# Optimization experiments

Measured on AMD Instinct MI355X. Metric: run time of the kernel, lower is better.

The kernel has to match this reference:

```python
import jax, jax.numpy as jnp
import numpy as np

EMBED = 256
HID = 256          # LSTM hidden_dim
ENC = 256          # enc_hid_dim
DEC = 256          # dec_hid_dim (attention)


def setup_inputs() -> dict:
    key = jax.random.key(0)
    ks = jax.random.split(key, 8)
    T, B, S = 256, 128, 512
    sc = 0.05
    return {
        "tgt": jax.random.normal(ks[0], (T, B, EMBED), dtype=jnp.float32),
        "memory": jax.random.normal(ks[1], (S, B, ENC), dtype=jnp.float32),
        # attention: Linear(enc+dec -> dec), input cat order = (hidden, encoder)
        "W_attn": jax.random.normal(ks[2], (DEC, DEC + ENC), dtype=jnp.float32) * sc,
        "b_attn": jnp.zeros((DEC,), dtype=jnp.float32),
        # LSTM (1 layer): input = embed + enc = 512, gates order i,f,g,o
        "W_ih": jax.random.normal(ks[3], (4 * HID, EMBED + ENC), dtype=jnp.float32) * sc,
        "W_hh": jax.random.normal(ks[4], (4 * HID, HID), dtype=jnp.float32) * sc,
        "b_ih": jnp.zeros((4 * HID,), dtype=jnp.float32),
        "b_hh": jnp.zeros((4 * HID,), dtype=jnp.float32),
    }


def _decode_scan(tgt, memory, W_attn, b_attn, W_ih, W_hh, b_ih, b_hh):
    T, B, _ = tgt.shape
    mem_bt = jnp.transpose(memory, (1, 0, 2))           # [B, S, ENC]
    # split attention weight by cat order (hidden first, then encoder)
    W_h = W_attn[:, :DEC]                               # [DEC, DEC]
    W_m = W_attn[:, DEC:]                               # [DEC, ENC]
    # precompute the memory side of the attention projection once
    mem_proj = jnp.einsum('bse,de->bsd', mem_bt, W_m) + b_attn  # [B, S, DEC]

    def step(carry, emb_t):
        h, c = carry                                    # [B, HID] each
        # Bahdanau attention: tanh(W[h; m]) summed over feature dim, softmax over S
        energy = jnp.tanh(mem_proj + (h @ W_h.T)[:, None, :])    # [B, S, DEC]
        attn = jax.nn.softmax(energy.sum(-1), axis=1)            # [B, S]
        ctx = jnp.einsum('bs,bse->be', attn, mem_bt)             # [B, ENC]
        x = jnp.concatenate([emb_t, ctx], axis=-1)               # [B, EMBED+ENC]
        gates = x @ W_ih.T + h @ W_hh.T + (b_ih + b_hh)          # [B, 4H]
        i, f, g, o = jnp.split(gates, 4, axis=-1)
        i, f, o = jax.nn.sigmoid(i), jax.nn.sigmoid(f), jax.nn.sigmoid(o)
        c_new = f * c + i * jnp.tanh(g)
        h_new = o * jnp.tanh(c_new)
        return (h_new, c_new), h_new

    h0 = jnp.zeros((B, HID), dtype=tgt.dtype)
    c0 = jnp.zeros((B, HID), dtype=tgt.dtype)
    # loop runs for t = 1..T-1; outputs[0] stays zero, tgt[0] unused
    _, outs = jax.lax.scan(step, (h0, c0), tgt[1:])              # [T-1, B, HID]
    return jnp.concatenate([jnp.zeros((1, B, HID), dtype=tgt.dtype), outs], axis=0)


def reference(tgt, memory, W_attn, b_attn, W_ih, W_hh, b_ih, b_hh):
    return _decode_scan(tgt, memory, W_attn, b_attn, W_ih, W_hh, b_ih, b_hh)
```

## Files before the change

kernel.cpp:

```cpp
#include <hip/hip_runtime.h>
#include <string.h>

#define T_STEPS 256
#define B_SZ    128
#define S_SZ    512
#define D_SZ    256
#define NG      1024

__device__ float g_proj[(size_t)B_SZ * S_SZ * 256];
__device__ float g_E[(size_t)T_STEPS * B_SZ * 1024];
__device__ float g_WihT[512 * 1024];
__device__ float g_WhhT[256 * 1024];
__device__ float g_WhT [256 * 256];
__device__ float g_WmT [256 * 256];
__device__ float g_bias[1024];

__device__ __forceinline__ float tanh_f(float x){
    float r = __expf(2.f * x);
    return 1.f - 2.f / (r + 1.f);
}
__device__ __forceinline__ float sigm_f(float x){
    return 1.f / (1.f + __expf(-x));
}


__global__ void pack_attn(const float* __restrict__ W_attn){
    int id = blockIdx.x * 256 + threadIdx.x;
    int d = id >> 8, k = id & 255;
    g_WhT[k * 256 + d] = W_attn[d * 512 + k];
    g_WmT[k * 256 + d] = W_attn[d * 512 + 256 + k];
}

__global__ void pack_wih(const float* __restrict__ W){
    int id = blockIdx.x * 256 + threadIdx.x;
    int j = id >> 9, k = id & 511;
    g_WihT[k * 1024 + j] = W[id];
}
__global__ void pack_whh(const float* __restrict__ W){
    int id = blockIdx.x * 256 + threadIdx.x;
    int j = id >> 8, k = id & 255;
    g_WhhT[k * 1024 + j] = W[id];
}
__global__ void pack_bias(const float* __restrict__ bih, const float* __restrict__ bhh){
    int j = blockIdx.x * 256 + threadIdx.x;
    g_bias[j] = bih[j] + bhh[j];
}

#define PBM 64
#define PBN 64
#define PBK 32
__global__ __launch_bounds__(256) void mem_proj_gemm(
        const float* __restrict__ memory,
        const float* __restrict__ b_attn){
    __shared__ float As[PBK][PBM + 1];
    __shared__ float Bs[PBK][PBN + 1];
    int tid = threadIdx.x;
    int tm = tid >> 4, tn = tid & 15;
    int row0 = blockIdx.x * PBM;
    int col0 = blockIdx.y * PBN;
    float acc[4][4] = {};
    for (int k0 = 0; k0 < 256; k0 += PBK){
        int m = tid >> 2, kq = tid & 3;
        int r  = row0 + m;
        int bb = r >> 9, ss = r & 511;
        const float* ap = memory + ((size_t)ss * B_SZ + bb) * 256 + k0 + kq * 8;
        #pragma unroll
        for (int i = 0; i < 8; ++i) As[kq * 8 + i][m] = ap[i];
        int kk = tid >> 3, dq = tid & 7;
        const float* bp = g_WmT + (size_t)(k0 + kk) * 256 + col0 + dq * 8;
        #pragma unroll
        for (int i = 0; i < 8; ++i) Bs[kk][dq * 8 + i] = bp[i];
        __syncthreads();
        #pragma unroll
        for (int k2 = 0; k2 < PBK; ++k2){
            float a[4], bb2[4];
            #pragma unroll
            for (int i = 0; i < 4; ++i) a[i]   = As[k2][tm * 4 + i];
            #pragma unroll
            for (int i = 0; i < 4; ++i) bb2[i] = Bs[k2][tn * 4 + i];
            #pragma unroll
            for (int i = 0; i < 4; ++i)
                #pragma unroll
                for (int j = 0; j < 4; ++j) acc[i][j] += a[i] * bb2[j];
        }
        __syncthreads();
    }
    #pragma unroll
    for (int i = 0; i < 4; ++i){
        int r = row0 + tm * 4 + i;
        float* pp = g_proj + (size_t)r * 256 + col0 + tn * 4;
        #pragma unroll
        for (int j = 0; j < 4; ++j)
            pp[j] = acc[i][j] + b_attn[col0 + tn * 4 + j];
    }
}

__global__ __launch_bounds__(256) void emb_gemm(
        const float* __restrict__ tgt){
    __shared__ float As[PBK][PBM + 1];
    __shared__ float Bs[PBK][PBN + 1];
    int tid = threadIdx.x;
    int tm = tid >> 4, tn = tid & 15;
    int row0 = blockIdx.x * PBM;
    int col0 = blockIdx.y * PBN;
    float acc[4][4] = {};
    for (int k0 = 0; k0 < 256; k0 += PBK){
        int m = tid >> 2, kq = tid & 3;
        const float* ap = tgt + (size_t)(row0 + m) * 256 + k0 + kq * 8;
        #pragma unroll
        for (int i = 0; i < 8; ++i) As[kq * 8 + i][m] = ap[i];
        int kk = tid >> 3, dq = tid & 7;
        const float* bp = g_WihT + (size_t)(k0 + kk) * 1024 + col0 + dq * 8;
        #pragma unroll
        for (int i = 0; i < 8; ++i) Bs[kk][dq * 8 + i] = bp[i];
        __syncthreads();
        #pragma unroll
        for (int k2 = 0; k2 < PBK; ++k2){
            float a[4], bb2[4];
            #pragma unroll
            for (int i = 0; i < 4; ++i) a[i]   = As[k2][tm * 4 + i];
            #pragma unroll
            for (int i = 0; i < 4; ++i) bb2[i] = Bs[k2][tn * 4 + i];
            #pragma unroll
            for (int i = 0; i < 4; ++i)
                #pragma unroll
                for (int j = 0; j < 4; ++j) acc[i][j] += a[i] * bb2[j];
        }
        __syncthreads();
    }
    #pragma unroll
    for (int i = 0; i < 4; ++i){
        int r = row0 + tm * 4 + i;
        float* pp = g_E + (size_t)r * 1024 + col0 + tn * 4;
        #pragma unroll
        for (int j = 0; j < 4; ++j)
            __builtin_nontemporal_store(acc[i][j], pp + j);
    }
}

__global__ __launch_bounds__(1024) void decode_scan(
        const float* __restrict__ memory,
        float* __restrict__ out)
{
    const int b    = blockIdx.x;
    const int tid  = threadIdx.x;
    const int lane = tid & 63;
    const int wave = tid >> 6;

    __shared__ __align__(16) float h_s[256];
    __shared__ __align__(16) float c_s[256];
    __shared__ __align__(16) float hWh_part[4][256];
    __shared__ __align__(16) float hWh[256];
    __shared__ __align__(16) float e_s[512];
    __shared__ __align__(16) float attn[512];
    __shared__ __align__(16) float ctx_part[16][256];
    __shared__ __align__(16) float ctx_s[256];
    __shared__ __align__(16) float g_part[4][1024];
    __shared__ __align__(16) float gates[1024];

    if (tid < 256){
        h_s[tid] = 0.f; c_s[tid] = 0.f;
        __builtin_nontemporal_store(0.f, out + (size_t)b * 256 + tid);
    }
    __syncthreads();

    const float* projb = g_proj + (size_t)b * S_SZ * 256;
    const float* memb  = memory + (size_t)b * 256;

    for (int t = 1; t < T_STEPS; ++t){
        {
            int d = tid & 255, kq = tid >> 8;
            float acc = 0.f;
            const float* wp = g_WhT + (size_t)(kq * 64) * 256 + d;
            #pragma unroll 8
            for (int k = 0; k < 64; ++k)
                acc += h_s[kq * 64 + k] * wp[(size_t)k * 256];
            hWh_part[kq][d] = acc;
        }
        __syncthreads();
        if (tid < 256)
            hWh[tid] = hWh_part[0][tid] + hWh_part[1][tid] + hWh_part[2][tid] + hWh_part[3][tid];
        __syncthreads();

        {
            float4 hv = ((const float4*)hWh)[lane];
            for (int i = 0; i < 32; ++i){
                int s = wave * 32 + i;
                float4 p = ((const float4*)(projb + (size_t)s * 256))[lane];
                float v = tanh_f(p.x + hv.x) + tanh_f(p.y + hv.y)
                        + tanh_f(p.z + hv.z) + tanh_f(p.w + hv.w);
                #pragma unroll
                for (int m = 32; m; m >>= 1) v += __shfl_xor(v, m, 64);
                if (lane == 0) e_s[s] = v;
            }
        }
        __syncthreads();

        if (wave == 0){
            float v[8]; float mx = -1e30f;
            #pragma unroll
            for (int i = 0; i < 8; ++i){ v[i] = e_s[lane + 64 * i]; mx = fmaxf(mx, v[i]); }
            #pragma unroll
            for (int m = 32; m; m >>= 1) mx = fmaxf(mx, __shfl_xor(mx, m, 64));
            float zs = 0.f;
            #pragma unroll
            for (int i = 0; i < 8; ++i){ v[i] = __expf(v[i] - mx); zs += v[i]; }
            #pragma unroll
            for (int m = 32; m; m >>= 1) zs += __shfl_xor(zs, m, 64);
            float inv = 1.f / zs;
            #pragma unroll
            for (int i = 0; i < 8; ++i) attn[lane + 64 * i] = v[i] * inv;
        }
        __syncthreads();

        {
            int e4 = tid & 63, sq = tid >> 6;
            float a0=0.f, a1=0.f, a2=0.f, a3=0.f;
            const float* mp = memb + (size_t)(sq * 32) * 32768 + 4 * e4;
            #pragma unroll 4
            for (int s = 0; s < 32; ++s){
                float av = attn[sq * 32 + s];
                float4 w = *(const float4*)(mp + (size_t)s * 32768);
                a0 += av * w.x; a1 += av * w.y;
                a2 += av * w.z; a3 += av * w.w;
            }
            float4 r; r.x=a0; r.y=a1; r.z=a2; r.w=a3;
            ((float4*)ctx_part[sq])[e4] = r;
        }
        __syncthreads();
        if (tid < 256){
            float s = 0.f;
            #pragma unroll
            for (int g = 0; g < 16; ++g) s += ctx_part[g][tid];
            ctx_s[tid] = s;
        }
        __syncthreads();

        {
            int jq = tid & 255, kh = tid >> 8;
            float a0=0.f, a1=0.f, a2=0.f, a3=0.f;
            const float* src;
            const float* wp;
            if (kh < 2){
                src = ctx_s + kh * 128;
                wp  = g_WihT + (size_t)(256 + kh * 128) * 1024 + 4 * jq;
            } else {
                src = h_s + (kh - 2) * 128;
                wp  = g_WhhT + (size_t)((kh - 2) * 128) * 1024 + 4 * jq;
            }
            #pragma unroll 4
            for (int k = 0; k < 128; ++k){
                float xv = src[k];
                float4 w = *(const float4*)(wp + (size_t)k * 1024);
                a0 += xv * w.x; a1 += xv * w.y;
                a2 += xv * w.z; a3 += xv * w.w;
            }
            float4 r; r.x=a0; r.y=a1; r.z=a2; r.w=a3;
            ((float4*)g_part[kh])[jq] = r;
        }
        __syncthreads();
        {
            const float* Erow = g_E + ((size_t)t * B_SZ + b) * 1024;
            float ev = __builtin_nontemporal_load(Erow + tid);
            gates[tid] = g_part[0][tid] + g_part[1][tid] + g_part[2][tid]
                       + g_part[3][tid] + ev + g_bias[tid];
        }
        __syncthreads();

        if (tid < 256){
            float ig = sigm_f(gates[tid]);
            float fg = sigm_f(gates[256 + tid]);
            float gg = tanh_f(gates[512 + tid]);
            float og = sigm_f(gates[768 + tid]);
            float cn = fg * c_s[tid] + ig * gg;
            float hn = og * tanh_f(cn);
            c_s[tid] = cn; h_s[tid] = hn;
            __builtin_nontemporal_store(hn, out + ((size_t)t * B_SZ + b) * 256 + tid);
        }
        __syncthreads();
    }
}

extern "C" void kernel_launch(void* const* d_in, const int* in_sizes, int n_in,
                              void* d_out, int out_size, void* d_ws, size_t ws_size,
                              hipStream_t stream){
    const float* tgt    = (const float*)d_in[0];
    const float* memory = (const float*)d_in[1];
    const float* W_attn = (const float*)d_in[2];
    const float* b_attn = (const float*)d_in[3];
    const float* W_ih   = (const float*)d_in[4];
    const float* W_hh   = (const float*)d_in[5];
    const float* b_ih   = (const float*)d_in[6];
    const float* b_hh   = (const float*)d_in[7];
    float* out = (float*)d_out;
    (void)d_ws; (void)ws_size; (void)in_sizes; (void)n_in; (void)out_size;

    pack_attn<<<256, 256, 0, stream>>>(W_attn);
    pack_wih<<<2048, 256, 0, stream>>>(W_ih);
    pack_whh<<<1024, 256, 0, stream>>>(W_hh);
    pack_bias<<<4, 256, 0, stream>>>(b_ih, b_hh);
    emb_gemm<<<dim3(512, 16), 256, 0, stream>>>(tgt);
    mem_proj_gemm<<<dim3(1024, 4), 256, 0, stream>>>(memory, b_attn);
    decode_scan<<<128, 1024, 0, stream>>>(memory, out);
}
```

Baseline: 14.70 ms.

## Split each batch row's decode across two cooperating blocks with flag sync

The recurrent decode kernel now uses two 512-thread blocks per batch element. Each block handles half of the source positions for attention energy and context, and half of the gate columns. Partial energies, contexts and gates are exchanged through global memory, with three spin-flag pair syncs per timestep. The aim is to use 256 CUs instead of 128 and halve per-block work. The cost is cross-block synchronization latency, and the spin cap means results could silently go wrong if the partner block is not co-resident.

```diff
diff --git a/kernel.cpp b/kernel.cpp
--- a/kernel.cpp
+++ b/kernel.cpp
@@ -6,6 +6,8 @@
 #define S_SZ    512
 #define D_SZ    256
 #define NG      1024
+
+#define SPIN_CAP 50000
 
 __device__ float g_proj[(size_t)B_SZ * S_SZ * 256];
 __device__ float g_E[(size_t)T_STEPS * B_SZ * 1024];
@@ -15,6 +17,11 @@
 __device__ float g_WmT [256 * 256];
 __device__ float g_bias[1024];
 
+__device__ float g_ex_e   [B_SZ][512];
+__device__ float g_ex_ctx [B_SZ][2][256];
+__device__ float g_ex_gate[B_SZ][1024];
+__device__ int   g_flags  [2 * B_SZ];
+
 __device__ __forceinline__ float tanh_f(float x){
     float r = __expf(2.f * x);
     return 1.f - 2.f / (r + 1.f);
@@ -22,7 +29,6 @@
 __device__ __forceinline__ float sigm_f(float x){
     return 1.f / (1.f + __expf(-x));
 }
-
 
 __global__ void pack_attn(const float* __restrict__ W_attn){
     int id = blockIdx.x * 256 + threadIdx.x;
@@ -30,7 +36,6 @@
     g_WhT[k * 256 + d] = W_attn[d * 512 + k];
     g_WmT[k * 256 + d] = W_attn[d * 512 + 256 + k];
 }
-
 __global__ void pack_wih(const float* __restrict__ W){
     int id = blockIdx.x * 256 + threadIdx.x;
     int j = id >> 9, k = id & 511;
@@ -44,6 +49,7 @@
 __global__ void pack_bias(const float* __restrict__ bih, const float* __restrict__ bhh){
     int j = blockIdx.x * 256 + threadIdx.x;
     g_bias[j] = bih[j] + bhh[j];
+    if (j < 2 * B_SZ) g_flags[j] = 0;
 }
 
 #define PBM 64
@@ -138,61 +144,94 @@
     }
 }
 
-__global__ __launch_bounds__(1024) void decode_scan(
+__device__ __forceinline__ void pair_sync(int myid, int partner, int target, int* dead){
+    __syncthreads();
+    if (threadIdx.x == 0 && !*dead){
+        __hip_atomic_store(&g_flags[myid], target, __ATOMIC_RELEASE, __HIP_MEMORY_SCOPE_AGENT);
+        int spins = 0;
+        while (__hip_atomic_load(&g_flags[partner], __ATOMIC_RELAXED, __HIP_MEMORY_SCOPE_AGENT) < target){
+            __builtin_amdgcn_s_sleep(2);
+            if (++spins > SPIN_CAP){ *dead = 1; break; }
+        }
+    }
+    __syncthreads();
+}
+
+__global__ __launch_bounds__(512) void decode_scan(
         const float* __restrict__ memory,
         float* __restrict__ out)
 {
-    const int b    = blockIdx.x;
+    const int bid  = blockIdx.x;
+    const int b    = bid >> 1;
+    const int p    = bid & 1;
+    const int partner = bid ^ 1;
     const int tid  = threadIdx.x;
     const int lane = tid & 63;
     const int wave = tid >> 6;
+    const int s0   = p * 256;
+    const int j0   = p * 512;
 
     __shared__ __align__(16) float h_s[256];
     __shared__ __align__(16) float c_s[256];
-    __shared__ __align__(16) float hWh_part[4][256];
-    __shared__ __align__(16) float hWh[256];
+    __shared__ __align__(16) float hWh_part[2][256];
     __shared__ __align__(16) float e_s[512];
     __shared__ __align__(16) float attn[512];
-    __shared__ __align__(16) float ctx_part[16][256];
+    __shared__ __align__(16) float ctx_part[8][256];
     __shared__ __align__(16) float ctx_s[256];
-    __shared__ __align__(16) float g_part[4][1024];
+    __shared__ __align__(16) float g_part[4][512];
     __shared__ __align__(16) float gates[1024];
+    __shared__ int s_dead;
 
     if (tid < 256){
         h_s[tid] = 0.f; c_s[tid] = 0.f;
-        __builtin_nontemporal_store(0.f, out + (size_t)b * 256 + tid);
-    }
+        if (p == 0)
+            __builtin_nontemporal_store(0.f, out + (size_t)b * 256 + tid);
+    }
+    if (tid == 0) s_dead = 0;
     __syncthreads();
 
-    const float* projb = g_proj + (size_t)b * S_SZ * 256;
+    const float* projb = g_proj + ((size_t)b * S_SZ + s0) * 256;
     const float* memb  = memory + (size_t)b * 256;
 
+    int ctr = 0;
     for (int t = 1; t < T_STEPS; ++t){
         {
             int d = tid & 255, kq = tid >> 8;
             float acc = 0.f;
-            const float* wp = g_WhT + (size_t)(kq * 64) * 256 + d;
+            const float* wp = g_WhT + (size_t)(kq * 128) * 256 + d;
             #pragma unroll 8
-            for (int k = 0; k < 64; ++k)
-                acc += h_s[kq * 64 + k] * wp[(size_t)k * 256];
+            for (int k = 0; k < 128; ++k)
+                acc += h_s[kq * 128 + k] * wp[(size_t)k * 256];
             hWh_part[kq][d] = acc;
         }
         __syncthreads();
-        if (tid < 256)
-            hWh[tid] = hWh_part[0][tid] + hWh_part[1][tid] + hWh_part[2][tid] + hWh_part[3][tid];
-        __syncthreads();
-
-        {
-            float4 hv = ((const float4*)hWh)[lane];
+
+        {
+            float4 p0 = ((const float4*)hWh_part[0])[lane];
+            float4 p1 = ((const float4*)hWh_part[1])[lane];
+            float4 hv;
+            hv.x = p0.x + p1.x; hv.y = p0.y + p1.y;
+            hv.z = p0.z + p1.z; hv.w = p0.w + p1.w;
+            #pragma unroll 4
             for (int i = 0; i < 32; ++i){
-                int s = wave * 32 + i;
-                float4 p = ((const float4*)(projb + (size_t)s * 256))[lane];
-                float v = tanh_f(p.x + hv.x) + tanh_f(p.y + hv.y)
-                        + tanh_f(p.z + hv.z) + tanh_f(p.w + hv.w);
+                int sl = wave * 32 + i;
+                float4 q = ((const float4*)(projb + (size_t)sl * 256))[lane];
+                float v = tanh_f(q.x + hv.x) + tanh_f(q.y + hv.y)
+                        + tanh_f(q.z + hv.z) + tanh_f(q.w + hv.w);
                 #pragma unroll
                 for (int m = 32; m; m >>= 1) v += __shfl_xor(v, m, 64);
-                if (lane == 0) e_s[s] = v;
+                if (lane == 0) e_s[s0 + sl] = v;
             }
+        }
+        __syncthreads();
+        if (tid < 256)
+            __hip_atomic_store(&g_ex_e[b][s0 + tid], e_s[s0 + tid],
+                               __ATOMIC_RELAXED, __HIP_MEMORY_SCOPE_AGENT);
+        pair_sync(bid, partner, ++ctr, &s_dead);
+        if (tid < 256){
+            int so = s0 ^ 256;
+            e_s[so + tid] = __hip_atomic_load(&g_ex_e[b][so + tid],
+                               __ATOMIC_RELAXED, __HIP_MEMORY_SCOPE_AGENT);
         }
         __syncthreads();
 
@@ -216,10 +255,10 @@
         {
             int e4 = tid & 63, sq = tid >> 6;
             float a0=0.f, a1=0.f, a2=0.f, a3=0.f;
-            const float* mp = memb + (size_t)(sq * 32) * 32768 + 4 * e4;
+            const float* mp = memb + (size_t)(s0 + sq * 32) * 32768 + 4 * e4;
             #pragma unroll 4
             for (int s = 0; s < 32; ++s){
-                float av = attn[sq * 32 + s];
+                float av = attn[s0 + sq * 32 + s];
                 float4 w = *(const float4*)(mp + (size_t)s * 32768);
                 a0 += av * w.x; a1 += av * w.y;
                 a2 += av * w.z; a3 += av * w.w;
@@ -231,22 +270,30 @@
         if (tid < 256){
             float s = 0.f;
             #pragma unroll
-            for (int g = 0; g < 16; ++g) s += ctx_part[g][tid];
-            ctx_s[tid] = s;
-        }
-        __syncthreads();
-
-        {
-            int jq = tid & 255, kh = tid >> 8;
+            for (int g = 0; g < 8; ++g) s += ctx_part[g][tid];
+            ctx_part[0][tid] = s;
+            __hip_atomic_store(&g_ex_ctx[b][p][tid], s,
+                               __ATOMIC_RELAXED, __HIP_MEMORY_SCOPE_AGENT);
+        }
+        pair_sync(bid, partner, ++ctr, &s_dead);
+        if (tid < 256){
+            float o = __hip_atomic_load(&g_ex_ctx[b][p ^ 1][tid],
+                               __ATOMIC_RELAXED, __HIP_MEMORY_SCOPE_AGENT);
+            ctx_s[tid] = ctx_part[0][tid] + o;
+        }
+        __syncthreads();
+
+        {
+            int jq = tid & 127, kh = tid >> 7;
             float a0=0.f, a1=0.f, a2=0.f, a3=0.f;
             const float* src;
             const float* wp;
             if (kh < 2){
                 src = ctx_s + kh * 128;
-                wp  = g_WihT + (size_t)(256 + kh * 128) * 1024 + 4 * jq;
+                wp  = g_WihT + (size_t)(256 + kh * 128) * 1024 + j0 + 4 * jq;
             } else {
                 src = h_s + (kh - 2) * 128;
-                wp  = g_WhhT + (size_t)((kh - 2) * 128) * 1024 + 4 * jq;
+                wp  = g_WhhT + (size_t)((kh - 2) * 128) * 1024 + j0 + 4 * jq;
             }
             #pragma unroll 4
             for (int k = 0; k < 128; ++k){
@@ -260,10 +307,19 @@
         }
         __syncthreads();
         {
-            const float* Erow = g_E + ((size_t)t * B_SZ + b) * 1024;
+            const float* Erow = g_E + ((size_t)t * B_SZ + b) * 1024 + j0;
             float ev = __builtin_nontemporal_load(Erow + tid);
-            gates[tid] = g_part[0][tid] + g_part[1][tid] + g_part[2][tid]
-                       + g_part[3][tid] + ev + g_bias[tid];
+            float gv = g_part[0][tid] + g_part[1][tid] + g_part[2][tid]
+                     + g_part[3][tid] + ev + g_bias[j0 + tid];
+            gates[j0 + tid] = gv;
+            __hip_atomic_store(&g_ex_gate[b][j0 + tid], gv,
+                               __ATOMIC_RELAXED, __HIP_MEMORY_SCOPE_AGENT);
+        }
+        pair_sync(bid, partner, ++ctr, &s_dead);
+        {
+            int jo = j0 ^ 512;
+            gates[jo + tid] = __hip_atomic_load(&g_ex_gate[b][jo + tid],
+                               __ATOMIC_RELAXED, __HIP_MEMORY_SCOPE_AGENT);
         }
         __syncthreads();
 
@@ -275,7 +331,8 @@
             float cn = fg * c_s[tid] + ig * gg;
             float hn = og * tanh_f(cn);
             c_s[tid] = cn; h_s[tid] = hn;
-            __builtin_nontemporal_store(hn, out + ((size_t)t * B_SZ + b) * 256 + tid);
+            if (p == 0)
+                __builtin_nontemporal_store(hn, out + ((size_t)t * B_SZ + b) * 256 + tid);
         }
         __syncthreads();
     }
@@ -301,5 +358,5 @@
     pack_bias<<<4, 256, 0, stream>>>(b_ih, b_hh);
     emb_gemm<<<dim3(512, 16), 256, 0, stream>>>(tgt);
     mem_proj_gemm<<<dim3(1024, 4), 256, 0, stream>>>(memory, b_attn);
-    decode_scan<<<128, 1024, 0, stream>>>(memory, out);
-}
+    decode_scan<<<256, 512, 0, stream>>>(memory, out);
+}
```

After: 15.83 ms. 7.7% more time.

## Transpose attention projection to d-major layout and drop per-position wave reductions

Applied to the files above, without the earlier changes.

The precomputed memory projection is now stored transposed per batch as [d][s], so each wave handles 16 feature rows and lanes cover 8 sequence positions each. Per-position 64-lane shuffle reductions are replaced by per-lane accumulation, plus a cross-wave sum through a new 32KB shared buffer. The GEMM reads W_attn directly, so the packed WmT copy is removed. The gate-input load from g_E is issued at the top of each step to hide its latency. The extra shared memory and extra barrier may reduce occupancy or add sync cost.

```diff
diff --git a/kernel.cpp b/kernel.cpp
--- a/kernel.cpp
+++ b/kernel.cpp
@@ -7,12 +7,11 @@
 #define D_SZ    256
 #define NG      1024
 
-__device__ float g_proj[(size_t)B_SZ * S_SZ * 256];
+__device__ float g_projT[(size_t)B_SZ * 256 * 512];
 __device__ float g_E[(size_t)T_STEPS * B_SZ * 1024];
 __device__ float g_WihT[512 * 1024];
 __device__ float g_WhhT[256 * 1024];
 __device__ float g_WhT [256 * 256];
-__device__ float g_WmT [256 * 256];
 __device__ float g_bias[1024];
 
 __device__ __forceinline__ float tanh_f(float x){
@@ -22,15 +21,12 @@
 __device__ __forceinline__ float sigm_f(float x){
     return 1.f / (1.f + __expf(-x));
 }
-
 
 __global__ void pack_attn(const float* __restrict__ W_attn){
     int id = blockIdx.x * 256 + threadIdx.x;
     int d = id >> 8, k = id & 255;
     g_WhT[k * 256 + d] = W_attn[d * 512 + k];
-    g_WmT[k * 256 + d] = W_attn[d * 512 + 256 + k];
-}
-
+}
 __global__ void pack_wih(const float* __restrict__ W){
     int id = blockIdx.x * 256 + threadIdx.x;
     int j = id >> 9, k = id & 511;
@@ -46,65 +42,65 @@
     g_bias[j] = bih[j] + bhh[j];
 }
 
-#define PBM 64
-#define PBN 64
-#define PBK 32
-__global__ __launch_bounds__(256) void mem_proj_gemm(
+__global__ __launch_bounds__(256) void mem_projT_gemm(
         const float* __restrict__ memory,
+        const float* __restrict__ W_attn,
         const float* __restrict__ b_attn){
-    __shared__ float As[PBK][PBM + 1];
-    __shared__ float Bs[PBK][PBN + 1];
+    __shared__ float As[32][65];
+    __shared__ float Bs[32][65];
     int tid = threadIdx.x;
     int tm = tid >> 4, tn = tid & 15;
-    int row0 = blockIdx.x * PBM;
-    int col0 = blockIdx.y * PBN;
+    int row0 = blockIdx.x * 64;
+    int col0 = blockIdx.y * 64;
     float acc[4][4] = {};
-    for (int k0 = 0; k0 < 256; k0 += PBK){
+    for (int k0 = 0; k0 < 256; k0 += 32){
         int m = tid >> 2, kq = tid & 3;
-        int r  = row0 + m;
+        const float* ap = W_attn + (size_t)(row0 + m) * 512 + 256 + k0 + kq * 8;
+        #pragma unroll
+        for (int i = 0; i < 8; ++i) As[kq * 8 + i][m] = ap[i];
+        int r  = col0 + m;
         int bb = r >> 9, ss = r & 511;
-        const float* ap = memory + ((size_t)ss * B_SZ + bb) * 256 + k0 + kq * 8;
-        #pragma unroll
-        for (int i = 0; i < 8; ++i) As[kq * 8 + i][m] = ap[i];
-        int kk = tid >> 3, dq = tid & 7;
-        const float* bp = g_WmT + (size_t)(k0 + kk) * 256 + col0 + dq * 8;
-        #pragma unroll
-        for (int i = 0; i < 8; ++i) Bs[kk][dq * 8 + i] = bp[i];
-        __syncthreads();
-        #pragma unroll
-        for (int k2 = 0; k2 < PBK; ++k2){
-            float a[4], bb2[4];
-            #pragma unroll
-            for (int i = 0; i < 4; ++i) a[i]   = As[k2][tm * 4 + i];
-            #pragma unroll
-            for (int i = 0; i < 4; ++i) bb2[i] = Bs[k2][tn * 4 + i];
+        const float* bp = memory + ((size_t)ss * B_SZ + bb) * 256 + k0 + kq * 8;
+        #pragma unroll
+        for (int i = 0; i < 8; ++i) Bs[kq * 8 + i][m] = bp[i];
+        __syncthreads();
+        #pragma unroll
+        for (int k2 = 0; k2 < 32; ++k2){
+            float a[4], bv[4];
+            #pragma unroll
+            for (int i = 0; i < 4; ++i) a[i]  = As[k2][tm * 4 + i];
+            #pragma unroll
+            for (int i = 0; i < 4; ++i) bv[i] = Bs[k2][tn * 4 + i];
             #pragma unroll
             for (int i = 0; i < 4; ++i)
                 #pragma unroll
-                for (int j = 0; j < 4; ++j) acc[i][j] += a[i] * bb2[j];
-        }
-        __syncthreads();
-    }
+                for (int j = 0; j < 4; ++j) acc[i][j] += a[i] * bv[j];
+        }
+        __syncthreads();
+    }
+    int bb_o = col0 >> 9;
+    int s_o  = (col0 & 511) + tn * 4;
     #pragma unroll
     for (int i = 0; i < 4; ++i){
-        int r = row0 + tm * 4 + i;
-        float* pp = g_proj + (size_t)r * 256 + col0 + tn * 4;
+        int d = row0 + tm * 4 + i;
+        float bi = b_attn[d];
+        float* pp = g_projT + ((size_t)bb_o * 256 + d) * 512 + s_o;
         #pragma unroll
         for (int j = 0; j < 4; ++j)
-            pp[j] = acc[i][j] + b_attn[col0 + tn * 4 + j];
+            pp[j] = acc[i][j] + bi;
     }
 }
 
 __global__ __launch_bounds__(256) void emb_gemm(
         const float* __restrict__ tgt){
-    __shared__ float As[PBK][PBM + 1];
-    __shared__ float Bs[PBK][PBN + 1];
+    __shared__ float As[32][65];
+    __shared__ float Bs[32][65];
     int tid = threadIdx.x;
     int tm = tid >> 4, tn = tid & 15;
-    int row0 = blockIdx.x * PBM;
-    int col0 = blockIdx.y * PBN;
+    int row0 = blockIdx.x * 64;
+    int col0 = blockIdx.y * 64;
     float acc[4][4] = {};
-    for (int k0 = 0; k0 < 256; k0 += PBK){
+    for (int k0 = 0; k0 < 256; k0 += 32){
         int m = tid >> 2, kq = tid & 3;
         const float* ap = tgt + (size_t)(row0 + m) * 256 + k0 + kq * 8;
         #pragma unroll
@@ -115,16 +111,16 @@
         for (int i = 0; i < 8; ++i) Bs[kk][dq * 8 + i] = bp[i];
         __syncthreads();
         #pragma unroll
-        for (int k2 = 0; k2 < PBK; ++k2){
-            float a[4], bb2[4];
-            #pragma unroll
-            for (int i = 0; i < 4; ++i) a[i]   = As[k2][tm * 4 + i];
-            #pragma unroll
-            for (int i = 0; i < 4; ++i) bb2[i] = Bs[k2][tn * 4 + i];
+        for (int k2 = 0; k2 < 32; ++k2){
+            float a[4], bv[4];
+            #pragma unroll
+            for (int i = 0; i < 4; ++i) a[i]  = As[k2][tm * 4 + i];
+            #pragma unroll
+            for (int i = 0; i < 4; ++i) bv[i] = Bs[k2][tn * 4 + i];
             #pragma unroll
             for (int i = 0; i < 4; ++i)
                 #pragma unroll
-                for (int j = 0; j < 4; ++j) acc[i][j] += a[i] * bb2[j];
+                for (int j = 0; j < 4; ++j) acc[i][j] += a[i] * bv[j];
         }
         __syncthreads();
     }
@@ -151,6 +147,7 @@
     __shared__ __align__(16) float c_s[256];
     __shared__ __align__(16) float hWh_part[4][256];
     __shared__ __align__(16) float hWh[256];
+    __shared__ __align__(16) float e_part[16][512];
     __shared__ __align__(16) float e_s[512];
     __shared__ __align__(16) float attn[512];
     __shared__ __align__(16) float ctx_part[16][256];
@@ -164,10 +161,13 @@
     }
     __syncthreads();
 
-    const float* projb = g_proj + (size_t)b * S_SZ * 256;
-    const float* memb  = memory + (size_t)b * 256;
+    const float* projTb = g_projT + (size_t)b * 256 * 512;
+    const float* memb   = memory + (size_t)b * 256;
 
     for (int t = 1; t < T_STEPS; ++t){
+        float ev = __builtin_nontemporal_load(
+                        g_E + ((size_t)t * B_SZ + b) * 1024 + tid);
+
         {
             int d = tid & 255, kq = tid >> 8;
             float acc = 0.f;
@@ -183,16 +183,28 @@
         __syncthreads();
 
         {
-            float4 hv = ((const float4*)hWh)[lane];
-            for (int i = 0; i < 32; ++i){
-                int s = wave * 32 + i;
-                float4 p = ((const float4*)(projb + (size_t)s * 256))[lane];
-                float v = tanh_f(p.x + hv.x) + tanh_f(p.y + hv.y)
-                        + tanh_f(p.z + hv.z) + tanh_f(p.w + hv.w);
-                #pragma unroll
-                for (int m = 32; m; m >>= 1) v += __shfl_xor(v, m, 64);
-                if (lane == 0) e_s[s] = v;
+            const float* pT = projTb + (size_t)(wave * 16) * 512 + lane * 8;
+            float4 aA = {0.f,0.f,0.f,0.f}, aB = {0.f,0.f,0.f,0.f};
+            #pragma unroll 2
+            for (int dd = 0; dd < 16; ++dd){
+                float hw = hWh[wave * 16 + dd];
+                const float4* rp = (const float4*)(pT + (size_t)dd * 512);
+                float4 q1 = rp[0];
+                float4 q2 = rp[1];
+                aA.x += tanh_f(q1.x + hw); aA.y += tanh_f(q1.y + hw);
+                aA.z += tanh_f(q1.z + hw); aA.w += tanh_f(q1.w + hw);
+                aB.x += tanh_f(q2.x + hw); aB.y += tanh_f(q2.y + hw);
+                aB.z += tanh_f(q2.z + hw); aB.w += tanh_f(q2.w + hw);
             }
+            float4* ep = (float4*)&e_part[wave][lane * 8];
+            ep[0] = aA; ep[1] = aB;
+        }
+        __syncthreads();
+        if (tid < 512){
+            float v = 0.f;
+            #pragma unroll
+            for (int w2 = 0; w2 < 16; ++w2) v += e_part[w2][tid];
+            e_s[tid] = v;
         }
         __syncthreads();
 
@@ -259,12 +271,8 @@
             ((float4*)g_part[kh])[jq] = r;
         }
         __syncthreads();
-        {
-            const float* Erow = g_E + ((size_t)t * B_SZ + b) * 1024;
-            float ev = __builtin_nontemporal_load(Erow + tid);
-            gates[tid] = g_part[0][tid] + g_part[1][tid] + g_part[2][tid]
-                       + g_part[3][tid] + ev + g_bias[tid];
-        }
+        gates[tid] = g_part[0][tid] + g_part[1][tid] + g_part[2][tid]
+                   + g_part[3][tid] + ev + g_bias[tid];
         __syncthreads();
 
         if (tid < 256){
@@ -300,6 +308,6 @@
     pack_whh<<<1024, 256, 0, stream>>>(W_hh);
     pack_bias<<<4, 256, 0, stream>>>(b_ih, b_hh);
     emb_gemm<<<dim3(512, 16), 256, 0, stream>>>(tgt);
-    mem_proj_gemm<<<dim3(1024, 4), 256, 0, stream>>>(memory, b_attn);
+    mem_projT_gemm<<<dim3(4, 1024), 256, 0, stream>>>(memory, W_attn, b_attn);
     decode_scan<<<128, 1024, 0, stream>>>(memory, out);
 }
```

Measured after the change: 12.97 ms. 1.13x faster.
